# Optimization experiments

Hardware: AMD Instinct MI355X
Metric: run time of the kernel (lower is better)

## Reference

```python
import jax, jax.numpy as jnp
import numpy as np

B, T, V, S, I, G = 2, 4096, 1024, 256, 2048, 128


def setup_inputs() -> dict:
    key = jax.random.key(0)
    ks = jax.random.split(key, 10)
    n = lambda k, shape, std: jax.random.normal(k, shape, dtype=jnp.float32) * std
    return {
        "x": jax.random.normal(ks[0], (B, T, V), dtype=jnp.float32),
        # shared CausalMemory projections (torch Linear weight layout [out,in])
        "Wq": n(ks[1], (S, V), 0.02),
        "Wk": n(ks[2], (S, V), 0.02),
        "Wv": n(ks[3], (S, V), 0.02),
        "Wo": n(ks[4], (V, S), 0.02),
        # Delta
        "delta_logits": jnp.full((V,), 4.0, dtype=jnp.float32),
        "delta_scale": jnp.float32(0.1),
        # Theta / Gamma decay params
        "theta_decay": jnp.float32(4.0),
        "theta_scale": jnp.float32(0.1),
        "gamma_decay": jnp.float32(1.0),
        "gamma_scale": jnp.float32(0.1),
        # Alpha gate
        "alpha_down": n(ks[5], (G, V), 0.02),
        "alpha_up": n(ks[6], (V, G), 0.01),
        "alpha_up_b": jnp.full((V,), 2.0, dtype=jnp.float32),
        # Beta MLP
        "beta_down": n(ks[7], (I, V), 0.02),
        "beta_up": n(ks[8], (V, I), 0.02),
        "beta_bias": jnp.zeros((I,), dtype=jnp.float32),
        "beta_scale": jnp.float32(0.1),
    }


def _rmsnorm(x):
    eps = jnp.finfo(x.dtype).eps
    return x * jax.lax.rsqrt(jnp.mean(x * x, axis=-1, keepdims=True) + eps)


def _delta(x, decay_logits, scale):
    # causal EMA via weighted cumsum, matching torch reference exactly
    t = x.shape[1]
    decay = jax.nn.sigmoid(decay_logits)
    log_decay = jnp.log(jnp.clip(decay, 1e-06))
    steps = jnp.arange(t, dtype=x.dtype)[::-1]            # [T]
    w = jnp.exp(steps[:, None] * log_decay[None, :])      # [T,V]
    cum = jnp.cumsum(x * w[None], axis=1)
    cum = jnp.concatenate([jnp.zeros_like(cum[:, :1]), cum[:, :-1]], axis=1)
    return cum / jnp.clip(w[None], 1e-08) * scale


def _memory(x, Wq, Wk, Wv, Wo, decay_logit, scale):
    t = x.shape[1]
    q = x @ Wq.T
    k = x @ Wk.T
    v = x @ Wv.T
    scores = jnp.einsum("btd,bsd->bts", q, k)             # [B,T,T]
    decay = jax.nn.sigmoid(decay_logit)
    pos = jnp.arange(t)
    diff = pos[None, :] - pos[:, None]                    # j - i
    w = decay ** jnp.clip(diff.astype(x.dtype) - 1.0, 0.0, None) * (diff > 0)
    retrieved = jnp.einsum("bts,bsd->btd", scores * w[None], v)
    return (retrieved @ Wo.T) * scale


def _alpha(x, down, up, up_b):
    gate = jax.nn.sigmoid((x @ down.T) @ up.T + up_b)
    return x * gate


def _beta(x, down, up, bias, scale):
    h = jax.nn.gelu(x @ down.T + bias, approximate=False)
    return (h @ up.T) * scale


def reference(x, Wq, Wk, Wv, Wo, delta_logits, delta_scale, theta_decay,
              theta_scale, gamma_decay, gamma_scale, alpha_down, alpha_up,
              alpha_up_b, beta_down, beta_up, beta_bias, beta_scale):
    x = x + _delta(_rmsnorm(x), delta_logits, delta_scale)
    x = x + _memory(_rmsnorm(x), Wq, Wk, Wv, Wo, theta_decay, theta_scale)
    x = _alpha(x, alpha_down, alpha_up, alpha_up_b)
    x = x + _beta(_rmsnorm(x), beta_down, beta_up, beta_bias, beta_scale)
    x = x + _memory(_rmsnorm(x), Wq, Wk, Wv, Wo, gamma_decay, gamma_scale)
    return x
```

## Files before the change

### kernel.cpp

```cpp
#include <hip/hip_runtime.h>

typedef __attribute__((ext_vector_type(8))) short s16x8;
typedef __attribute__((ext_vector_type(4))) float f32x4;
typedef unsigned short u16;

#define DEV __device__ __forceinline__

DEV u16 f2b(float f) {
  unsigned u = __builtin_bit_cast(unsigned, f);
  unsigned r = (u + 0x7FFFu + ((u >> 16) & 1u)) >> 16;
  return (u16)r;
}
DEV float b2f(u16 h) { return __builtin_bit_cast(float, (unsigned)h << 16); }
DEV f32x4 mfma16(s16x8 a, s16x8 b, f32x4 c) {
  return __builtin_amdgcn_mfma_f32_16x16x32_bf16(a, b, c, 0, 0, 0);
}
DEV float sigmoidf_(float x) { return 1.0f / (1.0f + expf(-x)); }

DEV void g2l16(const u16* g, u16* l) {
  __builtin_amdgcn_global_load_lds((const __attribute__((address_space(1))) void*)g,
                                   (__attribute__((address_space(3))) void*)l, 16, 0, 0);
}

#define BAR() __builtin_amdgcn_s_barrier()
#define WAITV8() asm volatile("s_waitcnt vmcnt(8)" ::: "memory")
#define WAITV4() asm volatile("s_waitcnt vmcnt(4)" ::: "memory")
#define WAITV0() asm volatile("s_waitcnt vmcnt(0)" ::: "memory")
#define WAITL0()                                         \
  do {                                                   \
    asm volatile("s_waitcnt lgkmcnt(0)" ::: "memory");   \
    __builtin_amdgcn_sched_barrier(0);                   \
  } while (0)

__global__ __launch_bounds__(256) void cast_all(
    const float* __restrict__ Wq, const float* __restrict__ Wk, const float* __restrict__ Wv,
    const float* __restrict__ Wo, const float* __restrict__ adw, const float* __restrict__ auw,
    const float* __restrict__ bdw, const float* __restrict__ buw,
    u16* __restrict__ Wqkvb, u16* __restrict__ Wob, u16* __restrict__ adb,
    u16* __restrict__ aub, u16* __restrict__ bdb, u16* __restrict__ bub) {
  const int b = blockIdx.x;
  const float* s;
  u16* d;
  int rb;
  if (b < 768) {
    s = (b < 256) ? Wq : (b < 512) ? Wk : Wv;
    rb = (b < 256) ? b : (b < 512) ? (b - 256) : (b - 512);
    d = Wqkvb + ((b < 256) ? 0 : (b < 512) ? 262144 : 524288);
  } else if (b < 1024) { s = Wo;  d = Wob; rb = b - 768; }
  else if (b < 1152)   { s = adw; d = adb; rb = b - 1024; }
  else if (b < 1280)   { s = auw; d = aub; rb = b - 1152; }
  else if (b < 3328)   { s = bdw; d = bdb; rb = b - 1280; }
  else                 { s = buw; d = bub; rb = b - 3328; }
  size_t i = ((size_t)rb * 256 + threadIdx.x) * 4;
  float4 v = *(const float4*)(s + i);
  ushort4 p; p.x = f2b(v.x); p.y = f2b(v.y); p.z = f2b(v.z); p.w = f2b(v.w);
  *(ushort4*)(d + i) = p;
}

__global__ __launch_bounds__(256) void rmsnorm_k(const float* __restrict__ x, u16* __restrict__ y) {
  const size_t row = blockIdx.x;
  const int tid = threadIdx.x;
  float4 v = ((const float4*)(x + row * 1024))[tid];
  float ss = v.x * v.x + v.y * v.y + v.z * v.z + v.w * v.w;
#pragma unroll
  for (int o = 32; o >= 1; o >>= 1) ss += __shfl_xor(ss, o);
  __shared__ float red[4];
  if ((tid & 63) == 0) red[tid >> 6] = ss;
  __syncthreads();
  float tot = red[0] + red[1] + red[2] + red[3];
  float rn = rsqrtf(tot * (1.0f / 1024.0f) + 1.1920929e-7f);
  ushort4 p;
  p.x = f2b(v.x * rn); p.y = f2b(v.y * rn); p.z = f2b(v.z * rn); p.w = f2b(v.w * rn);
  *(ushort4*)(y + row * 1024 + tid * 4) = p;
}

__global__ __launch_bounds__(256)
void delta_partial(const u16* __restrict__ y, const float* __restrict__ logits, float* __restrict__ Pp) {
  const int v = blockIdx.x * 256 + threadIdx.x;
  const int c = blockIdx.y, b = blockIdx.z;
  const float dec = sigmoidf_(logits[v]);
  const float ldc = logf(fmaxf(dec, 1e-6f));
  const float dc = expf(ldc);
  const u16* yp = y + ((size_t)b * 4096 + c * 128) * 1024 + v;
  float wv = expf((float)(4095 - (c * 128 + 127)) * ldc);
  float acc = 0.0f;
  for (int t = 127; t >= 0; --t) {
    acc += b2f(yp[(size_t)t * 1024]) * wv;
    wv *= dc;
  }
  Pp[((size_t)b * 32 + c) * 1024 + v] = acc;
}

__global__ __launch_bounds__(256) void delta_scan(float* __restrict__ Pp) {
  const int v = blockIdx.x * 256 + threadIdx.x;
  const int b = blockIdx.y;
  float run = 0.0f;
  for (int c = 0; c < 32; ++c) {
    size_t i = ((size_t)b * 32 + c) * 1024 + v;
    float t = Pp[i];
    Pp[i] = run;
    run += t;
  }
}

__global__ __launch_bounds__(256)
void delta_apply(const float* __restrict__ x0, const u16* __restrict__ y,
                 const float* __restrict__ logits, const float* __restrict__ scale_p,
                 const float* __restrict__ Pp, float* __restrict__ x1) {
  const int v = blockIdx.x * 256 + threadIdx.x;
  const int c = blockIdx.y, b = blockIdx.z;
  const float dec = sigmoidf_(logits[v]);
  const float ldc = logf(fmaxf(dec, 1e-6f));
  const float dc = expf(ldc);
  const float invd = expf(-ldc);
  const float sc = scale_p[0];
  float wv = expf((float)(4095 - c * 128) * ldc);
  float iw = expf(-(float)(4095 - c * 128) * ldc);
  float carry = Pp[((size_t)b * 32 + c) * 1024 + v];
  size_t base = ((size_t)b * 4096 + c * 128) * 1024 + v;
  for (int t = 0; t < 128; ++t) {
    size_t idx = base + (size_t)t * 1024;
    x1[idx] = x0[idx] + carry * fminf(iw, 1e8f) * sc;
    carry += b2f(y[idx]) * wv;
    wv *= invd;
    iw *= dc;
  }
}

template <int EPI>
__global__ __launch_bounds__(256, 4)
void pgemm_s(const u16* __restrict__ A, const u16* __restrict__ Bw,
             int M, int N, int K,
             u16* __restrict__ Cb,
             const float* __restrict__ Xin, float* __restrict__ Xout,
             u16* __restrict__ Xb16,
             const float* __restrict__ bias, const float* __restrict__ scale_p) {
  __shared__ u16 sm[17472];
  const int tid = threadIdx.x;
  const int wid = tid >> 6, lane = tid & 63;
  const int gx = gridDim.x;
  const int id = blockIdx.y * gx + blockIdx.x;
  const int q8 = (gx * gridDim.y) >> 3;
  const int nid = (id & 7) * q8 + (id >> 3);
  const int bx = nid % gx, by = nid / gx;
  const int n0 = bx * 128, m0 = by * 128;
  const int wm = (wid >> 1) * 64, wn = (wid & 1) * 64;
  const int lr = lane & 15, lkc = lane >> 4;
  const int sw = lr & 7;
  const int c0 = (lkc ^ sw) * 8, c1 = ((lkc + 4) ^ sw) * 8;
  const int NT = K >> 6;
  const int srow = lane >> 3;
  const int scol = ((lane & 7) ^ srow) * 8;
  const u16* Ag = A + (size_t)(m0 + wid * 8 + srow) * K + scol;
  const u16* Bg = Bw + (size_t)(n0 + wid * 8 + srow) * K + scol;
  u16* const As = sm;
  u16* const Bs = sm + 8192;

  f32x4 acc[4][4] = {};

  for (int t = 0; t < NT; ++t) {
    {
      const u16* ga = Ag + (size_t)t * 64;
      const u16* gb = Bg + (size_t)t * 64;
      u16* la = As + wid * 512;
      u16* lb = Bs + wid * 512;
#pragma unroll
      for (int c = 0; c < 4; ++c) {
        g2l16(ga + (size_t)c * 32 * K, la + c * 2048);
        g2l16(gb + (size_t)c * 32 * K, lb + c * 2048);
      }
    }
    __syncthreads();
    s16x8 af[4][2], bfr[2][2][2];
#pragma unroll
    for (int i = 0; i < 4; ++i) {
      int base = (wm + i * 16 + lr) * 64;
      af[i][0] = *(const s16x8*)&As[base + c0];
      af[i][1] = *(const s16x8*)&As[base + c1];
    }
#pragma unroll
    for (int h = 0; h < 2; ++h)
#pragma unroll
      for (int j = 0; j < 2; ++j) {
        int base = (wn + h * 32 + j * 16 + lr) * 64;
        bfr[h][j][0] = *(const s16x8*)&Bs[base + c0];
        bfr[h][j][1] = *(const s16x8*)&Bs[base + c1];
      }
#pragma unroll
    for (int i = 0; i < 4; ++i)
#pragma unroll
      for (int h = 0; h < 2; ++h)
#pragma unroll
        for (int j = 0; j < 2; ++j) {
          acc[i][h * 2 + j] = mfma16(af[i][0], bfr[h][j][0], acc[i][h * 2 + j]);
          acc[i][h * 2 + j] = mfma16(af[i][1], bfr[h][j][1], acc[i][h * 2 + j]);
        }
    __syncthreads();
  }

  float* tl = (float*)(void*)sm + wid * 1088;
  const float sc = (EPI == 2) ? scale_p[0] : 0.0f;
  float4 bpf = {0.0f, 0.0f, 0.0f, 0.0f};
  if constexpr (EPI == 3 || EPI == 4) bpf = *(const float4*)&bias[n0 + wn + lr * 4];
#pragma unroll
  for (int i = 0; i < 4; ++i) {
#pragma unroll
    for (int j = 0; j < 4; ++j)
#pragma unroll
      for (int r = 0; r < 4; ++r)
        tl[(lkc * 4 + r) * 68 + j * 16 + lr] = acc[i][j][r];
#pragma unroll
    for (int p = 0; p < 4; ++p) {
      const int row = p * 4 + lkc, nl = lr * 4;
      f32x4 v = *(const f32x4*)&tl[row * 68 + nl];
      const int m = m0 + wm + i * 16 + row;
      const int n = n0 + wn + nl;
      const size_t idx = (size_t)m * N + n;
      if constexpr (EPI == 0) {
        ushort4 o = {f2b(v[0]), f2b(v[1]), f2b(v[2]), f2b(v[3])};
        *(ushort4*)&Cb[idx] = o;
      } else if constexpr (EPI == 2) {
        float4 x = *(const float4*)&Xin[idx];
        float4 o = {x.x + v[0] * sc, x.y + v[1] * sc, x.z + v[2] * sc, x.w + v[3] * sc};
        *(float4*)&Xout[idx] = o;
        if (Xb16) {
          ushort4 ob = {f2b(o.x), f2b(o.y), f2b(o.z), f2b(o.w)};
          *(ushort4*)&Xb16[idx] = ob;
        }
      } else if constexpr (EPI == 3) {
        float g0 = v[0] + bpf.x, g1 = v[1] + bpf.y, g2 = v[2] + bpf.z, g3 = v[3] + bpf.w;
        ushort4 o;
        o.x = f2b(g0 * sigmoidf_(1.59576912f * fmaf(0.044715f * g0, g0 * g0, g0)));
        o.y = f2b(g1 * sigmoidf_(1.59576912f * fmaf(0.044715f * g1, g1 * g1, g1)));
        o.z = f2b(g2 * sigmoidf_(1.59576912f * fmaf(0.044715f * g2, g2 * g2, g2)));
        o.w = f2b(g3 * sigmoidf_(1.59576912f * fmaf(0.044715f * g3, g3 * g3, g3)));
        *(ushort4*)&Cb[idx] = o;
      } else {
        float4 x = *(const float4*)&Xin[idx];
        float4 o = {x.x * sigmoidf_(v[0] + bpf.x), x.y * sigmoidf_(v[1] + bpf.y),
                    x.z * sigmoidf_(v[2] + bpf.z), x.w * sigmoidf_(v[3] + bpf.w)};
        *(float4*)&Xout[idx] = o;
      }
    }
  }
}

template <int EPI>
__global__ __launch_bounds__(256, 2)
void pgemm_d(const u16* __restrict__ A, const u16* __restrict__ Bw,
             int M, int N, int K,
             u16* __restrict__ Cb,
             const float* __restrict__ Xin, float* __restrict__ Xout,
             u16* __restrict__ Xb16,
             const float* __restrict__ bias, const float* __restrict__ scale_p,
             u16* __restrict__ P1, u16* __restrict__ P2, u16* __restrict__ P3) {
  __shared__ u16 sm[32768];
  const int tid = threadIdx.x;
  const int wid = tid >> 6, lane = tid & 63;
  const int gx = gridDim.x;
  const int id = blockIdx.y * gx + blockIdx.x;
  const int q8 = (gx * gridDim.y) >> 3;
  const int nid = (id & 7) * q8 + (id >> 3);
  const int bx = nid % gx, by = nid / gx;
  const int n0 = bx * 128, m0 = by * 128;
  const int wm = (wid >> 1) * 64, wn = (wid & 1) * 64;
  const int lr = lane & 15, lkc = lane >> 4;
  const int sw = lr & 7;
  const int c0 = (lkc ^ sw) * 8, c1 = ((lkc + 4) ^ sw) * 8;
  const int NT = K >> 6;
  const int srow = lane >> 3;
  const int scol = ((lane & 7) ^ srow) * 8;
  const u16* Ag = A + (size_t)(m0 + wid * 8 + srow) * K + scol;
  const u16* Bg = Bw + (size_t)(n0 + wid * 8 + srow) * K + scol;
  u16* const AL0 = sm;          u16* const BL0 = sm + 8192;
  u16* const AL1 = sm + 16384;  u16* const BL1 = sm + 24576;

  f32x4 acc[4][4] = {};

  auto STA = [&](int tau) {
    const u16* g = Ag + (size_t)tau * 64;
    u16* l = ((tau & 1) ? AL1 : AL0) + wid * 512;
#pragma unroll
    for (int c = 0; c < 4; ++c) g2l16(g + (size_t)c * 32 * K, l + c * 2048);
  };
  auto STB = [&](int tau) {
    const u16* g = Bg + (size_t)tau * 64;
    u16* l = ((tau & 1) ? BL1 : BL0) + wid * 512;
#pragma unroll
    for (int c = 0; c < 4; ++c) g2l16(g + (size_t)c * 32 * K, l + c * 2048);
  };
  auto RDA = [&](int tau, s16x8 (&d)[4][2]) {
    const u16* Ab = (tau & 1) ? AL1 : AL0;
#pragma unroll
    for (int i = 0; i < 4; ++i) {
      int base = (wm + i * 16 + lr) * 64;
      d[i][0] = *(const s16x8*)&Ab[base + c0];
      d[i][1] = *(const s16x8*)&Ab[base + c1];
    }
  };
  auto RDB = [&](int tau, int h, s16x8 (&d)[2][2]) {
    const u16* Bb = (tau & 1) ? BL1 : BL0;
#pragma unroll
    for (int j = 0; j < 2; ++j) {
      int base = (wn + h * 32 + j * 16 + lr) * 64;
      d[j][0] = *(const s16x8*)&Bb[base + c0];
      d[j][1] = *(const s16x8*)&Bb[base + c1];
    }
  };
  auto MM = [&](s16x8 (&Ar)[4][2], s16x8 (&Br)[2][2], int jo) {
    __builtin_amdgcn_s_setprio(1);
#pragma unroll
    for (int i = 0; i < 4; ++i)
#pragma unroll
      for (int j = 0; j < 2; ++j) {
        acc[i][jo + j] = mfma16(Ar[i][0], Br[j][0], acc[i][jo + j]);
        acc[i][jo + j] = mfma16(Ar[i][1], Br[j][1], acc[i][jo + j]);
      }
    __builtin_amdgcn_s_setprio(0);
  };

  s16x8 Ae[4][2], Ao[4][2], B0r[2][2], B1r[2][2];
  STA(0); STB(0);
  if (NT > 1) { STA(1); STB(1); }
  WAITV8(); BAR();
  RDA(0, Ae); RDB(0, 0, B0r);

  for (int t = 0; t < NT; t += 2) {
    RDB(t, 1, B1r);
    if (t + 2 < NT) STA(t + 2);
    BAR(); WAITL0();
    MM(Ae, B0r, 0);
    BAR();
    if (t + 2 < NT) { STB(t + 2); WAITV8(); } else { WAITV0(); }
    BAR();
    if (t + 1 < NT) { RDA(t + 1, Ao); RDB(t + 1, 0, B0r); }
    WAITL0();
    MM(Ae, B1r, 2);
    BAR();
    if (t + 1 >= NT) break;
    RDB(t + 1, 1, B1r);
    if (t + 3 < NT) STA(t + 3);
    BAR(); WAITL0();
    MM(Ao, B0r, 0);
    BAR();
    if (t + 3 < NT) { STB(t + 3); WAITV8(); } else { WAITV0(); }
    BAR();
    if (t + 2 < NT) { RDA(t + 2, Ae); RDB(t + 2, 0, B0r); }
    WAITL0();
    MM(Ao, B1r, 2);
    BAR();
  }

  float* tl = (float*)(void*)sm + wid * 1088;

  if constexpr (EPI == 5) {
    if (bx < 4) {
      u16* dst = (bx < 2) ? Cb : P1;
      const int nb = (bx & 1) * 128;
#pragma unroll
      for (int i = 0; i < 4; ++i) {
#pragma unroll
        for (int j = 0; j < 4; ++j)
#pragma unroll
          for (int r = 0; r < 4; ++r)
            tl[(lkc * 4 + r) * 68 + j * 16 + lr] = acc[i][j][r];
#pragma unroll
        for (int p = 0; p < 4; ++p) {
          const int row = p * 4 + lkc, nl = lr * 4;
          f32x4 v = *(const f32x4*)&tl[row * 68 + nl];
          const int m = m0 + wm + i * 16 + row;
          ushort4 o = {f2b(v[0]), f2b(v[1]), f2b(v[2]), f2b(v[3])};
          *(ushort4*)&dst[(size_t)m * 256 + nb + wn + nl] = o;
        }
      }
      if (bx >= 2) {
        const float ld5 = logf(sigmoidf_(scale_p[0]));
        u16* CT = sm;
        __syncthreads();
#pragma unroll
        for (int i = 0; i < 4; ++i)
#pragma unroll
          for (int j = 0; j < 4; ++j)
#pragma unroll
            for (int r = 0; r < 4; ++r) {
              int ml = wm + i * 16 + lkc * 4 + r;
              int nl = wn + j * 16 + lr;
              float g = expf(ld5 * (float)(ml & 63));
              CT[nl * 136 + ml] = f2b(acc[i][j][r] * g);
            }
        __syncthreads();
        int d = tid >> 1, off = (tid & 1) * 64;
        size_t base = ((size_t)(m0 >> 12) * 256 + (bx - 2) * 128 + d) * 4096 + (m0 & 4095) + off;
#pragma unroll
        for (int p = 0; p < 8; ++p)
          *(uint4*)&P3[base + p * 8] = *(const uint4*)&CT[d * 136 + off + p * 8];
      }
    } else {
      u16* CT = sm;
      __syncthreads();
#pragma unroll
      for (int i = 0; i < 4; ++i)
#pragma unroll
        for (int j = 0; j < 4; ++j)
#pragma unroll
          for (int r = 0; r < 4; ++r) {
            int ml = wm + i * 16 + lkc * 4 + r;
            int nl = wn + j * 16 + lr;
            CT[nl * 136 + ml] = f2b(acc[i][j][r]);
          }
      __syncthreads();
      int d = tid >> 1, off = (tid & 1) * 64;
      size_t base = ((size_t)(m0 >> 12) * 256 + (bx - 4) * 128 + d) * 4096 + (m0 & 4095) + off;
#pragma unroll
      for (int p = 0; p < 8; ++p)
        *(uint4*)&P2[base + p * 8] = *(const uint4*)&CT[d * 136 + off + p * 8];
    }
  } else {
    const float sc = (EPI == 2) ? scale_p[0] : 0.0f;
    float4 bpf = {0.0f, 0.0f, 0.0f, 0.0f};
    if constexpr (EPI == 3 || EPI == 4) bpf = *(const float4*)&bias[n0 + wn + lr * 4];
#pragma unroll
    for (int i = 0; i < 4; ++i) {
#pragma unroll
      for (int j = 0; j < 4; ++j)
#pragma unroll
        for (int r = 0; r < 4; ++r)
          tl[(lkc * 4 + r) * 68 + j * 16 + lr] = acc[i][j][r];
#pragma unroll
      for (int p = 0; p < 4; ++p) {
        const int row = p * 4 + lkc, nl = lr * 4;
        f32x4 v = *(const f32x4*)&tl[row * 68 + nl];
        const int m = m0 + wm + i * 16 + row;
        const int n = n0 + wn + nl;
        const size_t idx = (size_t)m * N + n;
        if constexpr (EPI == 0) {
          ushort4 o = {f2b(v[0]), f2b(v[1]), f2b(v[2]), f2b(v[3])};
          *(ushort4*)&Cb[idx] = o;
        } else if constexpr (EPI == 2) {
          float4 x = *(const float4*)&Xin[idx];
          float4 o = {x.x + v[0] * sc, x.y + v[1] * sc, x.z + v[2] * sc, x.w + v[3] * sc};
          *(float4*)&Xout[idx] = o;
          if (Xb16) {
            ushort4 ob = {f2b(o.x), f2b(o.y), f2b(o.z), f2b(o.w)};
            *(ushort4*)&Xb16[idx] = ob;
          }
        } else if constexpr (EPI == 3) {
          float g0 = v[0] + bpf.x, g1 = v[1] + bpf.y, g2 = v[2] + bpf.z, g3 = v[3] + bpf.w;
          ushort4 o;
          o.x = f2b(g0 * sigmoidf_(1.59576912f * fmaf(0.044715f * g0, g0 * g0, g0)));
          o.y = f2b(g1 * sigmoidf_(1.59576912f * fmaf(0.044715f * g1, g1 * g1, g1)));
          o.z = f2b(g2 * sigmoidf_(1.59576912f * fmaf(0.044715f * g2, g2 * g2, g2)));
          o.w = f2b(g3 * sigmoidf_(1.59576912f * fmaf(0.044715f * g3, g3 * g3, g3)));
          *(ushort4*)&Cb[idx] = o;
        } else {
          float4 x = *(const float4*)&Xin[idx];
          float4 o = {x.x * sigmoidf_(v[0] + bpf.x), x.y * sigmoidf_(v[1] + bpf.y),
                      x.z * sigmoidf_(v[2] + bpf.z), x.w * sigmoidf_(v[3] + bpf.w)};
          *(float4*)&Xout[idx] = o;
        }
      }
    }
  }
}

__global__ __launch_bounds__(256, 2)
void chunk_G(const u16* __restrict__ vT, const u16* __restrict__ kTs, u16* __restrict__ Gp) {
  __shared__ u16 sm2[16384];
  const int c = blockIdx.x, eh = blockIdx.y >> 1, dh = blockIdx.y & 1, b = blockIdx.z;
  const int tid = threadIdx.x, wid = tid >> 6, lane = tid & 63;
  u16* AL = sm2; u16* BL = sm2 + 8192;
  const u16* As = vT + (size_t)(b * 256 + eh * 128) * 4096 + c * 64;
  const u16* Bs = kTs + (size_t)(b * 256 + dh * 128) * 4096 + c * 64;
  const int r8 = lane >> 3, sc8 = ((lane & 7) ^ (lane >> 3)) * 8;
#pragma unroll
  for (int p = 0; p < 4; ++p) {
    int ch = p * 4 + wid;
    int row = ch * 8 + r8;
    g2l16(As + (size_t)row * 4096 + sc8, AL + ch * 512);
    g2l16(Bs + (size_t)row * 4096 + sc8, BL + ch * 512);
  }
  __syncthreads();
  const int wm = (wid >> 1) * 64, wn = (wid & 1) * 64;
  const int lr = lane & 15, lkc = lane >> 4, sw = lr & 7;
  const int c0 = (lkc ^ sw) * 8, c1 = ((lkc + 4) ^ sw) * 8;
  s16x8 af[4][2], bf[4][2];
#pragma unroll
  for (int i = 0; i < 4; ++i) {
    int ba = (wm + i * 16 + lr) * 64;
    af[i][0] = *(const s16x8*)&AL[ba + c0];
    af[i][1] = *(const s16x8*)&AL[ba + c1];
    int bb = (wn + i * 16 + lr) * 64;
    bf[i][0] = *(const s16x8*)&BL[bb + c0];
    bf[i][1] = *(const s16x8*)&BL[bb + c1];
  }
  f32x4 acc[4][4] = {};
#pragma unroll
  for (int i = 0; i < 4; ++i)
#pragma unroll
    for (int j = 0; j < 4; ++j) {
      acc[i][j] = mfma16(af[i][0], bf[j][0], acc[i][j]);
      acc[i][j] = mfma16(af[i][1], bf[j][1], acc[i][j]);
    }
  u16* Gb = Gp + (size_t)(b * 64 + c) * 65536;
#pragma unroll
  for (int i = 0; i < 4; ++i)
#pragma unroll
    for (int j = 0; j < 4; ++j)
#pragma unroll
      for (int r = 0; r < 4; ++r) {
        int e = eh * 128 + wm + i * 16 + lkc * 4 + r;
        int d = dh * 128 + wn + j * 16 + lr;
        Gb[(size_t)e * 256 + d] = f2b(acc[i][j][r]);
      }
}

__global__ __launch_bounds__(256)
void scan_M(const u16* __restrict__ Gp, u16* __restrict__ Mb, const float* __restrict__ dlogit) {
  const int b = blockIdx.y;
  const size_t idx = (size_t)blockIdx.x * 256 + threadIdx.x;
  const float ld = logf(sigmoidf_(dlogit[0]));
  const float g64 = expf(64.0f * ld);
  const u16* G = Gp + (size_t)b * 64 * 65536 + idx;
  u16* M = Mb + (size_t)b * 64 * 65536 + idx;
  float m = 0.0f;
  M[(size_t)63 * 65536] = 0;
  float g = b2f(G[(size_t)63 * 65536]);
  for (int c = 62; c >= 0; --c) {
    float gn = 0.0f;
    if (c > 0) gn = b2f(G[(size_t)c * 65536]);
    m = g + g64 * m;
    M[(size_t)c * 65536] = f2b(m);
    g = gn;
  }
}

__global__ __launch_bounds__(256, 2)
void chunk_R(const u16* __restrict__ q, const u16* __restrict__ k,
             const u16* __restrict__ vT, const u16* __restrict__ Mb,
             u16* __restrict__ R, const float* __restrict__ dlogit) {
  __shared__ u16 qL[16384];
  __shared__ u16 shA[16384];
  const int c = blockIdx.x, eh = blockIdx.y, b = blockIdx.z;
  const int tid = threadIdx.x, wid = tid >> 6, lane = tid & 63;
  const float ld = logf(sigmoidf_(dlogit[0]));
  const int r8 = lane >> 3, sc8 = ((lane & 7) ^ (lane >> 3)) * 8;
  const int lr = lane & 15, lkc = lane >> 4, g4 = lkc * 4;
  const int sw = lr & 7;
  const int c0 = (lkc ^ sw) * 8, c1 = ((lkc + 4) ^ sw) * 8;

  const u16* qsrc = q + ((size_t)b * 4096 + c * 64) * 256;
  const u16* ksrc = k + ((size_t)b * 4096 + c * 64) * 256;
  const u16* msrc = Mb + ((size_t)(b * 64 + c) * 256 + eh * 128) * 256;
  const u16* vsrc = vT + (size_t)(b * 256 + eh * 128) * 4096 + c * 64;

#pragma unroll
  for (int kt = 0; kt < 4; ++kt)
#pragma unroll
    for (int p = 0; p < 2; ++p) {
      int ch = p * 4 + wid;
      int row = ch * 8 + r8;
      g2l16(qsrc + (size_t)row * 256 + kt * 64 + sc8, qL + kt * 4096 + ch * 512);
    }
#pragma unroll
  for (int p = 0; p < 4; ++p) {
    int ch = p * 4 + wid;
    int row = ch * 8 + r8;
    g2l16(msrc + (size_t)row * 256 + sc8, shA + ch * 512);
  }
  f32x4 accx[4][2] = {};
  for (int dt = 0; dt < 4; ++dt) {
    if (dt < 3) {
      u16* dst = shA + ((dt + 1) & 1) * 8192;
#pragma unroll
      for (int p = 0; p < 4; ++p) {
        int ch = p * 4 + wid;
        int row = ch * 8 + r8;
        g2l16(msrc + (size_t)row * 256 + (dt + 1) * 64 + sc8, dst + ch * 512);
      }
      WAITV4();
    } else {
      WAITV0();
    }
    BAR();
    const u16* mt = shA + (dt & 1) * 8192;
    const u16* qt = qL + dt * 4096;
    s16x8 aq[4][2], bm[2][2];
#pragma unroll
    for (int i = 0; i < 4; ++i) {
      int ba = (i * 16 + lr) * 64;
      aq[i][0] = *(const s16x8*)&qt[ba + c0];
      aq[i][1] = *(const s16x8*)&qt[ba + c1];
    }
#pragma unroll
    for (int j = 0; j < 2; ++j) {
      int ba = (wid * 32 + j * 16 + lr) * 64;
      bm[j][0] = *(const s16x8*)&mt[ba + c0];
      bm[j][1] = *(const s16x8*)&mt[ba + c1];
    }
#pragma unroll
    for (int i = 0; i < 4; ++i)
#pragma unroll
      for (int j = 0; j < 2; ++j) {
        accx[i][j] = mfma16(aq[i][0], bm[j][0], accx[i][j]);
        accx[i][j] = mfma16(aq[i][1], bm[j][1], accx[i][j]);
      }
    BAR();
  }
#pragma unroll
  for (int kt = 0; kt < 4; ++kt)
#pragma unroll
    for (int p = 0; p < 2; ++p) {
      int ch = p * 4 + wid;
      int row = ch * 8 + r8;
      g2l16(ksrc + (size_t)row * 256 + kt * 64 + sc8, shA + kt * 4096 + ch * 512);
    }
  __syncthreads();
  f32x4 accs[4] = {};
#pragma unroll
  for (int kt = 0; kt < 4; ++kt) {
    const u16* qt = qL + kt * 4096;
    const u16* klt = shA + kt * 4096;
    s16x8 aq[4][2], bk[2];
#pragma unroll
    for (int i = 0; i < 4; ++i) {
      int ba = (i * 16 + lr) * 64;
      aq[i][0] = *(const s16x8*)&qt[ba + c0];
      aq[i][1] = *(const s16x8*)&qt[ba + c1];
    }
    {
      int ba = (wid * 16 + lr) * 64;
      bk[0] = *(const s16x8*)&klt[ba + c0];
      bk[1] = *(const s16x8*)&klt[ba + c1];
    }
#pragma unroll
    for (int i = 0; i < 4; ++i) {
      accs[i] = mfma16(aq[i][0], bk[0], accs[i]);
      accs[i] = mfma16(aq[i][1], bk[1], accs[i]);
    }
  }
  __syncthreads();
  u16* PL = shA;
  u16* vTL = shA + 4608;
#pragma unroll
  for (int p = 0; p < 4; ++p) {
    int ch = p * 4 + wid;
    int row = ch * 8 + r8;
    g2l16(vsrc + (size_t)row * 4096 + sc8, vTL + ch * 512);
  }
#pragma unroll
  for (int i = 0; i < 4; ++i)
#pragma unroll
    for (int r = 0; r < 4; ++r) {
      int gi = i * 16 + g4 + r;
      int gj = wid * 16 + lr;
      float pw = (gj > gi) ? expf(ld * (float)(gj - gi - 1)) : 0.0f;
      PL[gi * 72 + gj] = f2b(accs[i][r] * pw);
    }
  __syncthreads();
  f32x4 acci[4][2] = {};
  {
    s16x8 pa[4][2], bv[2][2];
#pragma unroll
    for (int i = 0; i < 4; ++i) {
      pa[i][0] = *(const s16x8*)&PL[(i * 16 + lr) * 72 + lkc * 8];
      pa[i][1] = *(const s16x8*)&PL[(i * 16 + lr) * 72 + 32 + lkc * 8];
    }
#pragma unroll
    for (int j = 0; j < 2; ++j) {
      int ba = (wid * 32 + j * 16 + lr) * 64;
      bv[j][0] = *(const s16x8*)&vTL[ba + c0];
      bv[j][1] = *(const s16x8*)&vTL[ba + c1];
    }
#pragma unroll
    for (int i = 0; i < 4; ++i)
#pragma unroll
      for (int j = 0; j < 2; ++j) {
        acci[i][j] = mfma16(pa[i][0], bv[j][0], acci[i][j]);
        acci[i][j] = mfma16(pa[i][1], bv[j][1], acci[i][j]);
      }
  }
  u16* Ro = R + ((size_t)b * 4096 + c * 64) * 256 + eh * 128;
#pragma unroll
  for (int i = 0; i < 4; ++i)
#pragma unroll
    for (int r = 0; r < 4; ++r) {
      int gi = i * 16 + g4 + r;
      float xf = expf(ld * (float)(63 - gi));
#pragma unroll
      for (int j = 0; j < 2; ++j) {
        int ge = wid * 32 + j * 16 + lr;
        Ro[(size_t)gi * 256 + ge] = f2b(acci[i][j][r] + xf * accx[i][j][r]);
      }
    }
}

extern "C" void kernel_launch(void* const* d_in, const int* in_sizes, int n_in,
                              void* d_out, int out_size, void* d_ws, size_t ws_size,
                              hipStream_t stream) {
  const float* x0 = (const float*)d_in[0];
  const float* Wq = (const float*)d_in[1];
  const float* Wk = (const float*)d_in[2];
  const float* Wv = (const float*)d_in[3];
  const float* Wo = (const float*)d_in[4];
  const float* dlog = (const float*)d_in[5];
  const float* dscale = (const float*)d_in[6];
  const float* th_dec = (const float*)d_in[7];
  const float* th_sc = (const float*)d_in[8];
  const float* ga_dec = (const float*)d_in[9];
  const float* ga_sc = (const float*)d_in[10];
  const float* adw = (const float*)d_in[11];
  const float* auw = (const float*)d_in[12];
  const float* a_upb = (const float*)d_in[13];
  const float* bdw = (const float*)d_in[14];
  const float* buw = (const float*)d_in[15];
  const float* bbias = (const float*)d_in[16];
  const float* bscale = (const float*)d_in[17];

  char* w = (char*)d_ws;
  float* xA = (float*)w;
  u16* y = (u16*)(w + 33554432);
  u16* xb = (u16*)(w + 50331648);
  u16* qb = (u16*)(w + 67108864);
  u16* kb = (u16*)(w + 71303168);
  u16* vT = (u16*)(w + 75497472);
  u16* Rb = (u16*)(w + 79691776);
  u16* gb = (u16*)(w + 83886080);
  u16* hb = (u16*)(w + 85983232);
  u16* Gp = hb;
  u16* Mbuf = y;
  u16* kTs = xb;
  float* Pp = (float*)(w + 119537664);
  u16* Wqkvb = (u16*)(w + 119799808);
  u16* Wob = (u16*)(w + 121372672);
  u16* adb = (u16*)(w + 121896960);
  u16* aub = (u16*)(w + 122159104);
  u16* bdb = (u16*)(w + 122421248);
  u16* bub = (u16*)(w + 126615552);
  float* xB = (float*)d_out;

  cast_all<<<5376, 256, 0, stream>>>(Wq, Wk, Wv, Wo, adw, auw, bdw, buw,
                                     Wqkvb, Wob, adb, aub, bdb, bub);

  rmsnorm_k<<<8192, 256, 0, stream>>>(x0, y);
  delta_partial<<<dim3(4, 32, 2), 256, 0, stream>>>(y, dlog, Pp);
  delta_scan<<<dim3(4, 2), 256, 0, stream>>>(Pp);
  delta_apply<<<dim3(4, 32, 2), 256, 0, stream>>>(x0, y, dlog, dscale, Pp, xA);

  rmsnorm_k<<<8192, 256, 0, stream>>>(xA, y);
  pgemm_d<5><<<dim3(6, 64), 256, 0, stream>>>(y, Wqkvb, 8192, 768, 1024, qb, nullptr, nullptr, nullptr, nullptr, th_dec, kb, vT, kTs);
  chunk_G<<<dim3(64, 4, 2), 256, 0, stream>>>(vT, kTs, Gp);
  scan_M<<<dim3(256, 2), 256, 0, stream>>>(Gp, Mbuf, th_dec);
  chunk_R<<<dim3(64, 2, 2), 256, 0, stream>>>(qb, kb, vT, Mbuf, Rb, th_dec);
  pgemm_d<2><<<dim3(8, 64), 256, 0, stream>>>(Rb, Wob, 8192, 1024, 256, nullptr, xA, xB, xb, nullptr, th_sc, nullptr, nullptr, nullptr);

  pgemm_d<0><<<dim3(1, 64), 256, 0, stream>>>(xb, adb, 8192, 128, 1024, gb, nullptr, nullptr, nullptr, nullptr, nullptr, nullptr, nullptr, nullptr);
  pgemm_d<4><<<dim3(8, 64), 256, 0, stream>>>(gb, aub, 8192, 1024, 128, nullptr, xB, xA, nullptr, a_upb, nullptr, nullptr, nullptr, nullptr);

  rmsnorm_k<<<8192, 256, 0, stream>>>(xA, y);
  pgemm_s<3><<<dim3(16, 64), 256, 0, stream>>>(y, bdb, 8192, 2048, 1024, hb, nullptr, nullptr, nullptr, bbias, nullptr);
  pgemm_s<2><<<dim3(8, 64), 256, 0, stream>>>(hb, bub, 8192, 1024, 2048, nullptr, xA, xB, nullptr, nullptr, bscale);

  rmsnorm_k<<<8192, 256, 0, stream>>>(xB, y);
  pgemm_d<5><<<dim3(6, 64), 256, 0, stream>>>(y, Wqkvb, 8192, 768, 1024, qb, nullptr, nullptr, nullptr, nullptr, ga_dec, kb, vT, kTs);
  chunk_G<<<dim3(64, 4, 2), 256, 0, stream>>>(vT, kTs, Gp);
  scan_M<<<dim3(256, 2), 256, 0, stream>>>(Gp, Mbuf, ga_dec);
  chunk_R<<<dim3(64, 2, 2), 256, 0, stream>>>(qb, kb, vT, Mbuf, Rb, ga_dec);
  pgemm_d<2><<<dim3(8, 64), 256, 0, stream>>>(Rb, Wob, 8192, 1024, 256, nullptr, xB, xB, nullptr, nullptr, ga_sc, nullptr, nullptr, nullptr);
}
```

Before: 327.4 us.

## Emit bf16 residual copies from epilogues and halve delta chunk size

The delta_apply, alpha-gate, and beta GEMM epilogues now also write a bf16 copy of the residual stream. The following RMSNorm reads that half-width copy instead of the fp32 tensor, cutting its read traffic. The delta scan chunks shrink from 128 to 64 rows, doubling the blocks for more parallelism, and the partial-sum buffer moves into the gate buffer. RMSNorm statistics are now computed from bf16-rounded values, a small precision change, and each epilogue writes extra bytes.

```diff
diff --git a/kernel.cpp b/kernel.cpp
--- a/kernel.cpp
+++ b/kernel.cpp
@@ -74,6 +74,24 @@
   *(ushort4*)(y + row * 1024 + tid * 4) = p;
 }
 
+__global__ __launch_bounds__(256) void rmsnorm_b16(const u16* __restrict__ x, u16* __restrict__ y) {
+  const size_t row = blockIdx.x;
+  const int tid = threadIdx.x;
+  ushort4 h = ((const ushort4*)(x + row * 1024))[tid];
+  float v0 = b2f(h.x), v1 = b2f(h.y), v2 = b2f(h.z), v3 = b2f(h.w);
+  float ss = v0 * v0 + v1 * v1 + v2 * v2 + v3 * v3;
+#pragma unroll
+  for (int o = 32; o >= 1; o >>= 1) ss += __shfl_xor(ss, o);
+  __shared__ float red[4];
+  if ((tid & 63) == 0) red[tid >> 6] = ss;
+  __syncthreads();
+  float tot = red[0] + red[1] + red[2] + red[3];
+  float rn = rsqrtf(tot * (1.0f / 1024.0f) + 1.1920929e-7f);
+  ushort4 p;
+  p.x = f2b(v0 * rn); p.y = f2b(v1 * rn); p.z = f2b(v2 * rn); p.w = f2b(v3 * rn);
+  *(ushort4*)(y + row * 1024 + tid * 4) = p;
+}
+
 __global__ __launch_bounds__(256)
 void delta_partial(const u16* __restrict__ y, const float* __restrict__ logits, float* __restrict__ Pp) {
   const int v = blockIdx.x * 256 + threadIdx.x;
@@ -81,22 +99,22 @@
   const float dec = sigmoidf_(logits[v]);
   const float ldc = logf(fmaxf(dec, 1e-6f));
   const float dc = expf(ldc);
-  const u16* yp = y + ((size_t)b * 4096 + c * 128) * 1024 + v;
-  float wv = expf((float)(4095 - (c * 128 + 127)) * ldc);
+  const u16* yp = y + ((size_t)b * 4096 + c * 64) * 1024 + v;
+  float wv = expf((float)(4095 - (c * 64 + 63)) * ldc);
   float acc = 0.0f;
-  for (int t = 127; t >= 0; --t) {
+  for (int t = 63; t >= 0; --t) {
     acc += b2f(yp[(size_t)t * 1024]) * wv;
     wv *= dc;
   }
-  Pp[((size_t)b * 32 + c) * 1024 + v] = acc;
+  Pp[((size_t)b * 64 + c) * 1024 + v] = acc;
 }
 
 __global__ __launch_bounds__(256) void delta_scan(float* __restrict__ Pp) {
   const int v = blockIdx.x * 256 + threadIdx.x;
   const int b = blockIdx.y;
   float run = 0.0f;
-  for (int c = 0; c < 32; ++c) {
-    size_t i = ((size_t)b * 32 + c) * 1024 + v;
+  for (int c = 0; c < 64; ++c) {
+    size_t i = ((size_t)b * 64 + c) * 1024 + v;
     float t = Pp[i];
     Pp[i] = run;
     run += t;
@@ -106,7 +124,7 @@
 __global__ __launch_bounds__(256)
 void delta_apply(const float* __restrict__ x0, const u16* __restrict__ y,
                  const float* __restrict__ logits, const float* __restrict__ scale_p,
-                 const float* __restrict__ Pp, float* __restrict__ x1) {
+                 const float* __restrict__ Pp, float* __restrict__ x1, u16* __restrict__ x1b) {
   const int v = blockIdx.x * 256 + threadIdx.x;
   const int c = blockIdx.y, b = blockIdx.z;
   const float dec = sigmoidf_(logits[v]);
@@ -114,13 +132,15 @@
   const float dc = expf(ldc);
   const float invd = expf(-ldc);
   const float sc = scale_p[0];
-  float wv = expf((float)(4095 - c * 128) * ldc);
-  float iw = expf(-(float)(4095 - c * 128) * ldc);
-  float carry = Pp[((size_t)b * 32 + c) * 1024 + v];
-  size_t base = ((size_t)b * 4096 + c * 128) * 1024 + v;
-  for (int t = 0; t < 128; ++t) {
+  float wv = expf((float)(4095 - c * 64) * ldc);
+  float iw = expf(-(float)(4095 - c * 64) * ldc);
+  float carry = Pp[((size_t)b * 64 + c) * 1024 + v];
+  size_t base = ((size_t)b * 4096 + c * 64) * 1024 + v;
+  for (int t = 0; t < 64; ++t) {
     size_t idx = base + (size_t)t * 1024;
-    x1[idx] = x0[idx] + carry * fminf(iw, 1e8f) * sc;
+    float o = x0[idx] + carry * fminf(iw, 1e8f) * sc;
+    x1[idx] = o;
+    x1b[idx] = f2b(o);
     carry += b2f(y[idx]) * wv;
     wv *= invd;
     iw *= dc;
@@ -457,6 +477,10 @@
           float4 o = {x.x * sigmoidf_(v[0] + bpf.x), x.y * sigmoidf_(v[1] + bpf.y),
                       x.z * sigmoidf_(v[2] + bpf.z), x.w * sigmoidf_(v[3] + bpf.w)};
           *(float4*)&Xout[idx] = o;
+          if (Xb16) {
+            ushort4 ob = {f2b(o.x), f2b(o.y), f2b(o.z), f2b(o.w)};
+            *(ushort4*)&Xb16[idx] = ob;
+          }
         }
       }
     }
@@ -729,7 +753,7 @@
   u16* Gp = hb;
   u16* Mbuf = y;
   u16* kTs = xb;
-  float* Pp = (float*)(w + 119537664);
+  float* Pp = (float*)gb;
   u16* Wqkvb = (u16*)(w + 119799808);
   u16* Wob = (u16*)(w + 121372672);
   u16* adb = (u16*)(w + 121896960);
@@ -742,11 +766,11 @@
                                      Wqkvb, Wob, adb, aub, bdb, bub);
 
   rmsnorm_k<<<8192, 256, 0, stream>>>(x0, y);
-  delta_partial<<<dim3(4, 32, 2), 256, 0, stream>>>(y, dlog, Pp);
+  delta_partial<<<dim3(4, 64, 2), 256, 0, stream>>>(y, dlog, Pp);
   delta_scan<<<dim3(4, 2), 256, 0, stream>>>(Pp);
-  delta_apply<<<dim3(4, 32, 2), 256, 0, stream>>>(x0, y, dlog, dscale, Pp, xA);
-
-  rmsnorm_k<<<8192, 256, 0, stream>>>(xA, y);
+  delta_apply<<<dim3(4, 64, 2), 256, 0, stream>>>(x0, y, dlog, dscale, Pp, xA, xb);
+
+  rmsnorm_b16<<<8192, 256, 0, stream>>>(xb, y);
   pgemm_d<5><<<dim3(6, 64), 256, 0, stream>>>(y, Wqkvb, 8192, 768, 1024, qb, nullptr, nullptr, nullptr, nullptr, th_dec, kb, vT, kTs);
   chunk_G<<<dim3(64, 4, 2), 256, 0, stream>>>(vT, kTs, Gp);
   scan_M<<<dim3(256, 2), 256, 0, stream>>>(Gp, Mbuf, th_dec);
@@ -754,13 +778,13 @@
   pgemm_d<2><<<dim3(8, 64), 256, 0, stream>>>(Rb, Wob, 8192, 1024, 256, nullptr, xA, xB, xb, nullptr, th_sc, nullptr, nullptr, nullptr);
 
   pgemm_d<0><<<dim3(1, 64), 256, 0, stream>>>(xb, adb, 8192, 128, 1024, gb, nullptr, nullptr, nullptr, nullptr, nullptr, nullptr, nullptr, nullptr);
-  pgemm_d<4><<<dim3(8, 64), 256, 0, stream>>>(gb, aub, 8192, 1024, 128, nullptr, xB, xA, nullptr, a_upb, nullptr, nullptr, nullptr, nullptr);
-
-  rmsnorm_k<<<8192, 256, 0, stream>>>(xA, y);
+  pgemm_d<4><<<dim3(8, 64), 256, 0, stream>>>(gb, aub, 8192, 1024, 128, nullptr, xB, xA, xb, a_upb, nullptr, nullptr, nullptr, nullptr);
+
+  rmsnorm_b16<<<8192, 256, 0, stream>>>(xb, y);
   pgemm_s<3><<<dim3(16, 64), 256, 0, stream>>>(y, bdb, 8192, 2048, 1024, hb, nullptr, nullptr, nullptr, bbias, nullptr);
-  pgemm_s<2><<<dim3(8, 64), 256, 0, stream>>>(hb, bub, 8192, 1024, 2048, nullptr, xA, xB, nullptr, nullptr, bscale);
-
-  rmsnorm_k<<<8192, 256, 0, stream>>>(xB, y);
+  pgemm_s<2><<<dim3(8, 64), 256, 0, stream>>>(hb, bub, 8192, 1024, 2048, nullptr, xA, xB, xb, nullptr, bscale);
+
+  rmsnorm_b16<<<8192, 256, 0, stream>>>(xb, y);
   pgemm_d<5><<<dim3(6, 64), 256, 0, stream>>>(y, Wqkvb, 8192, 768, 1024, qb, nullptr, nullptr, nullptr, nullptr, ga_dec, kb, vT, kTs);
   chunk_G<<<dim3(64, 4, 2), 256, 0, stream>>>(vT, kTs, Gp);
   scan_M<<<dim3(256, 2), 256, 0, stream>>>(Gp, Mbuf, ga_dec);
```

Result: no change. 328.4 us (+0.3%).
